# Optimization experiments

Measured on AMD Instinct MI355X. Metric: run time of the kernel, lower is better.

## Reference

```python
import jax, jax.numpy as jnp
import numpy as np

B = 16384
C = 2048  # in_channel
OUT = 2   # out_channel


def setup_inputs() -> dict:
    key = jax.random.key(0)
    k1, k2, k3, k4, k5, k6, k7 = jax.random.split(key, 7)
    scale = 1.0 / np.sqrt(3 * C)  # torch Linear default init range
    return {
        "s_f": jax.random.normal(k1, (B, C), dtype=jnp.float32),
        "g_f": jax.random.normal(k2, (B, C), dtype=jnp.float32),
        "v_f": jax.random.normal(k3, (B, C), dtype=jnp.float32),
        "W_aff": jax.random.uniform(k4, (3 * C, 3), dtype=jnp.float32, minval=-scale, maxval=scale),
        "b_aff": jax.random.uniform(k5, (3,), dtype=jnp.float32, minval=-scale, maxval=scale),
        "W_cls": jax.random.uniform(k6, (3 * C, OUT), dtype=jnp.float32, minval=-scale, maxval=scale),
        "b_cls": jax.random.uniform(k7, (OUT,), dtype=jnp.float32, minval=-scale, maxval=scale),
    }


def reference(s_f, g_f, v_f, W_aff, b_aff, W_cls, b_cls):
    # Attention gating over the three modalities.
    x_att = jnp.concatenate([s_f, g_f, v_f], axis=1)          # [B, 3C]
    att = jax.nn.softmax(x_att @ W_aff + b_aff, axis=1)       # [B, 3]
    # diag(att[:, i]) @ f  ==  per-row scalar scaling (broadcast multiply).
    s = att[:, 0:1] * s_f
    g = att[:, 1:2] * g_f
    v = att[:, 2:3] * v_f
    x = jnp.concatenate([s, g, v], axis=1)                    # [B, 3C]
    return jax.nn.softmax(x @ W_cls + b_cls, axis=1)          # [B, OUT]
```

## Files before the change

### kernel.cpp

```cpp
#include <hip/hip_runtime.h>

#define B_ROWS 16384
#define C_DIM  2048
#define BLK    256
#define CHUNK  8
#define RPB    32
#define GROUP  8

#define DPP_ADD(v, ctrl, rmask) \
  v += __int_as_float(__builtin_amdgcn_update_dpp(0, __float_as_int(v), (ctrl), (rmask), 0xf, false))

__device__ __forceinline__ float wave_sum64(float v) {
  DPP_ADD(v, 0x111, 0xf);
  DPP_ADD(v, 0x112, 0xf);
  DPP_ADD(v, 0x114, 0xf);
  DPP_ADD(v, 0x118, 0xf);
  DPP_ADD(v, 0x142, 0xa);
  DPP_ADD(v, 0x143, 0xc);
  return v;
}

__global__ __launch_bounds__(BLK, 2)
void maff_fused(const float* __restrict__ s_f,
                const float* __restrict__ g_f,
                const float* __restrict__ v_f,
                const float* __restrict__ W_aff,
                const float* __restrict__ b_aff,
                const float* __restrict__ W_cls,
                const float* __restrict__ b_cls,
                float* __restrict__ out)
{
  const int t    = threadIdx.x;
  const int lane = t & 63;
  const int wave = t >> 6;
  const int c0   = t * CHUNK;

  float wa[3][CHUNK][3];
  float wc[3][CHUNK][2];
#pragma unroll
  for (int m = 0; m < 3; ++m) {
#pragma unroll
    for (int i = 0; i < CHUNK; ++i) {
      const int cc = m * C_DIM + c0 + i;
      wa[m][i][0] = W_aff[cc * 3 + 0];
      wa[m][i][1] = W_aff[cc * 3 + 1];
      wa[m][i][2] = W_aff[cc * 3 + 2];
      wc[m][i][0] = W_cls[cc * 2 + 0];
      wc[m][i][1] = W_cls[cc * 2 + 1];
    }
  }
  const float ba0 = b_aff[0], ba1 = b_aff[1], ba2 = b_aff[2];
  const float bc0 = b_cls[0], bc1 = b_cls[1];

  __shared__ float red[2][GROUP][4][9];

  const int row0 = blockIdx.x * RPB;

  float4 cs0, cs1, cg0, cg1, cv0, cv1;
  {
    const size_t off = (size_t)row0 * C_DIM + c0;
    cs0 = *(const float4*)(s_f + off); cs1 = *(const float4*)(s_f + off + 4);
    cg0 = *(const float4*)(g_f + off); cg1 = *(const float4*)(g_f + off + 4);
    cv0 = *(const float4*)(v_f + off); cv1 = *(const float4*)(v_f + off + 4);
  }

  for (int r = 0; r < RPB; ++r) {
    const int    pr   = (r + 1 < RPB) ? (row0 + r + 1) : row0;
    const size_t poff = (size_t)pr * C_DIM + c0;
    float4 ns0 = *(const float4*)(s_f + poff);
    float4 ns1 = *(const float4*)(s_f + poff + 4);
    float4 ng0 = *(const float4*)(g_f + poff);
    float4 ng1 = *(const float4*)(g_f + poff + 4);
    float4 nv0 = *(const float4*)(v_f + poff);
    float4 nv1 = *(const float4*)(v_f + poff + 4);

    float fs[CHUNK], fg[CHUNK], fv[CHUNK];
    fs[0]=cs0.x; fs[1]=cs0.y; fs[2]=cs0.z; fs[3]=cs0.w;
    fs[4]=cs1.x; fs[5]=cs1.y; fs[6]=cs1.z; fs[7]=cs1.w;
    fg[0]=cg0.x; fg[1]=cg0.y; fg[2]=cg0.z; fg[3]=cg0.w;
    fg[4]=cg1.x; fg[5]=cg1.y; fg[6]=cg1.z; fg[7]=cg1.w;
    fv[0]=cv0.x; fv[1]=cv0.y; fv[2]=cv0.z; fv[3]=cv0.w;
    fv[4]=cv1.x; fv[5]=cv1.y; fv[6]=cv1.z; fv[7]=cv1.w;

    float a0=0.f, a1=0.f, a2=0.f;
    float d00=0.f, d01=0.f, d10=0.f, d11=0.f, d20=0.f, d21=0.f;
#pragma unroll
    for (int i = 0; i < CHUNK; ++i) {
      a0 = fmaf(fs[i], wa[0][i][0], a0);
      a1 = fmaf(fs[i], wa[0][i][1], a1);
      a2 = fmaf(fs[i], wa[0][i][2], a2);
      a0 = fmaf(fg[i], wa[1][i][0], a0);
      a1 = fmaf(fg[i], wa[1][i][1], a1);
      a2 = fmaf(fg[i], wa[1][i][2], a2);
      a0 = fmaf(fv[i], wa[2][i][0], a0);
      a1 = fmaf(fv[i], wa[2][i][1], a1);
      a2 = fmaf(fv[i], wa[2][i][2], a2);
      d00 = fmaf(fs[i], wc[0][i][0], d00);
      d01 = fmaf(fs[i], wc[0][i][1], d01);
      d10 = fmaf(fg[i], wc[1][i][0], d10);
      d11 = fmaf(fg[i], wc[1][i][1], d11);
      d20 = fmaf(fv[i], wc[2][i][0], d20);
      d21 = fmaf(fv[i], wc[2][i][1], d21);
    }

    a0  = wave_sum64(a0);  a1  = wave_sum64(a1);  a2  = wave_sum64(a2);
    d00 = wave_sum64(d00); d01 = wave_sum64(d01);
    d10 = wave_sum64(d10); d11 = wave_sum64(d11);
    d20 = wave_sum64(d20); d21 = wave_sum64(d21);

    const int gslot = r & (GROUP - 1);
    const int gbuf  = (r / GROUP) & 1;
    if (lane == 63) {
      float* dst = &red[gbuf][gslot][wave][0];
      dst[0] = a0;  dst[1] = a1;  dst[2] = a2;
      dst[3] = d00; dst[4] = d01; dst[5] = d10;
      dst[6] = d11; dst[7] = d20; dst[8] = d21;
    }

    if (gslot == GROUP - 1) {
      __syncthreads();
      if (t < GROUP) {
        const float* q = &red[gbuf][t][0][0];
        float A0  = q[0] + q[ 9] + q[18] + q[27] + ba0;
        float A1  = q[1] + q[10] + q[19] + q[28] + ba1;
        float A2  = q[2] + q[11] + q[20] + q[29] + ba2;
        float D00 = q[3] + q[12] + q[21] + q[30];
        float D01 = q[4] + q[13] + q[22] + q[31];
        float D10 = q[5] + q[14] + q[23] + q[32];
        float D11 = q[6] + q[15] + q[24] + q[33];
        float D20 = q[7] + q[16] + q[25] + q[34];
        float D21 = q[8] + q[17] + q[26] + q[35];

        float mx = fmaxf(A0, fmaxf(A1, A2));
        float e0 = __expf(A0 - mx), e1 = __expf(A1 - mx), e2 = __expf(A2 - mx);
        float inv = 1.0f / (e0 + e1 + e2);
        float t0 = e0 * inv, t1 = e1 * inv, t2 = e2 * inv;

        float L0 = t0 * D00 + t1 * D10 + t2 * D20 + bc0;
        float L1 = t0 * D01 + t1 * D11 + t2 * D21 + bc1;
        float mm = fmaxf(L0, L1);
        float x0 = __expf(L0 - mm), x1 = __expf(L1 - mm);
        float is = 1.0f / (x0 + x1);

        const int row = row0 + (r - (GROUP - 1)) + t;
        *(float2*)(out + (size_t)row * 2) = make_float2(x0 * is, x1 * is);
      }
    }

    cs0 = ns0; cs1 = ns1; cg0 = ng0; cg1 = ng1; cv0 = nv0; cv1 = nv1;
  }
}

extern "C" void kernel_launch(void* const* d_in, const int* in_sizes, int n_in,
                              void* d_out, int out_size, void* d_ws, size_t ws_size,
                              hipStream_t stream) {
  const float* s_f   = (const float*)d_in[0];
  const float* g_f   = (const float*)d_in[1];
  const float* v_f   = (const float*)d_in[2];
  const float* W_aff = (const float*)d_in[3];
  const float* b_aff = (const float*)d_in[4];
  const float* W_cls = (const float*)d_in[5];
  const float* b_cls = (const float*)d_in[6];
  float* out = (float*)d_out;

  dim3 grid(B_ROWS / RPB);
  dim3 block(BLK);
  maff_fused<<<grid, block, 0, stream>>>(s_f, g_f, v_f, W_aff, b_aff, W_cls, b_cls, out);
}
```

Measured before the change: 364.2 us.

## Use 512-thread blocks with 4-wide chunks and 16 rows per block

Doubles the block to 512 threads, so each thread covers 4 channels instead of 8, and halves the rows per block to 16, which doubles the grid. Weight loads become vectorized float4 reads, and the cross-wave reduction loops over 8 waves. The aim is higher occupancy and more memory-level parallelism for this bandwidth-bound streaming kernel. In exchange, per-wave shuffle reductions and block barriers double relative to the data each thread handles.

```diff
diff --git a/kernel.cpp b/kernel.cpp
--- a/kernel.cpp
+++ b/kernel.cpp
@@ -2,10 +2,11 @@
 
 #define B_ROWS 16384
 #define C_DIM  2048
-#define BLK    256
-#define CHUNK  8
-#define RPB    32
+#define BLK    512
+#define CHUNK  4
+#define RPB    16
 #define GROUP  8
+#define NWAVE  (BLK / 64)
 
 #define DPP_ADD(v, ctrl, rmask) \
   v += __int_as_float(__builtin_amdgcn_update_dpp(0, __float_as_int(v), (ctrl), (rmask), 0xf, false))
@@ -20,7 +21,7 @@
   return v;
 }
 
-__global__ __launch_bounds__(BLK, 2)
+__global__ __launch_bounds__(BLK, 4)
 void maff_fused(const float* __restrict__ s_f,
                 const float* __restrict__ g_f,
                 const float* __restrict__ v_f,
@@ -35,72 +36,65 @@
   const int wave = t >> 6;
   const int c0   = t * CHUNK;
 
-  float wa[3][CHUNK][3];
-  float wc[3][CHUNK][2];
+  float waf[3][12];
+  float wcf[3][8];
 #pragma unroll
   for (int m = 0; m < 3; ++m) {
-#pragma unroll
-    for (int i = 0; i < CHUNK; ++i) {
-      const int cc = m * C_DIM + c0 + i;
-      wa[m][i][0] = W_aff[cc * 3 + 0];
-      wa[m][i][1] = W_aff[cc * 3 + 1];
-      wa[m][i][2] = W_aff[cc * 3 + 2];
-      wc[m][i][0] = W_cls[cc * 2 + 0];
-      wc[m][i][1] = W_cls[cc * 2 + 1];
-    }
+    const float4* pa = (const float4*)(W_aff + (size_t)(m * C_DIM + c0) * 3);
+    float4 a0 = pa[0], a1 = pa[1], a2 = pa[2];
+    waf[m][0]=a0.x; waf[m][1]=a0.y; waf[m][2]=a0.z; waf[m][3]=a0.w;
+    waf[m][4]=a1.x; waf[m][5]=a1.y; waf[m][6]=a1.z; waf[m][7]=a1.w;
+    waf[m][8]=a2.x; waf[m][9]=a2.y; waf[m][10]=a2.z; waf[m][11]=a2.w;
+    const float4* pc = (const float4*)(W_cls + (size_t)(m * C_DIM + c0) * 2);
+    float4 q0 = pc[0], q1 = pc[1];
+    wcf[m][0]=q0.x; wcf[m][1]=q0.y; wcf[m][2]=q0.z; wcf[m][3]=q0.w;
+    wcf[m][4]=q1.x; wcf[m][5]=q1.y; wcf[m][6]=q1.z; wcf[m][7]=q1.w;
   }
   const float ba0 = b_aff[0], ba1 = b_aff[1], ba2 = b_aff[2];
   const float bc0 = b_cls[0], bc1 = b_cls[1];
 
-  __shared__ float red[2][GROUP][4][9];
+  __shared__ float red[2][GROUP][NWAVE][9];
 
   const int row0 = blockIdx.x * RPB;
 
-  float4 cs0, cs1, cg0, cg1, cv0, cv1;
+  float4 cs, cg, cv;
   {
     const size_t off = (size_t)row0 * C_DIM + c0;
-    cs0 = *(const float4*)(s_f + off); cs1 = *(const float4*)(s_f + off + 4);
-    cg0 = *(const float4*)(g_f + off); cg1 = *(const float4*)(g_f + off + 4);
-    cv0 = *(const float4*)(v_f + off); cv1 = *(const float4*)(v_f + off + 4);
+    cs = *(const float4*)(s_f + off);
+    cg = *(const float4*)(g_f + off);
+    cv = *(const float4*)(v_f + off);
   }
 
   for (int r = 0; r < RPB; ++r) {
-    const int    pr   = (r + 1 < RPB) ? (row0 + r + 1) : row0;
+    const int    pr   = row0 + ((r + 1 < RPB) ? (r + 1) : r);
     const size_t poff = (size_t)pr * C_DIM + c0;
-    float4 ns0 = *(const float4*)(s_f + poff);
-    float4 ns1 = *(const float4*)(s_f + poff + 4);
-    float4 ng0 = *(const float4*)(g_f + poff);
-    float4 ng1 = *(const float4*)(g_f + poff + 4);
-    float4 nv0 = *(const float4*)(v_f + poff);
-    float4 nv1 = *(const float4*)(v_f + poff + 4);
+    float4 ns = *(const float4*)(s_f + poff);
+    float4 ng = *(const float4*)(g_f + poff);
+    float4 nv = *(const float4*)(v_f + poff);
 
-    float fs[CHUNK], fg[CHUNK], fv[CHUNK];
-    fs[0]=cs0.x; fs[1]=cs0.y; fs[2]=cs0.z; fs[3]=cs0.w;
-    fs[4]=cs1.x; fs[5]=cs1.y; fs[6]=cs1.z; fs[7]=cs1.w;
-    fg[0]=cg0.x; fg[1]=cg0.y; fg[2]=cg0.z; fg[3]=cg0.w;
-    fg[4]=cg1.x; fg[5]=cg1.y; fg[6]=cg1.z; fg[7]=cg1.w;
-    fv[0]=cv0.x; fv[1]=cv0.y; fv[2]=cv0.z; fv[3]=cv0.w;
-    fv[4]=cv1.x; fv[5]=cv1.y; fv[6]=cv1.z; fv[7]=cv1.w;
+    float fs[CHUNK] = {cs.x, cs.y, cs.z, cs.w};
+    float fg[CHUNK] = {cg.x, cg.y, cg.z, cg.w};
+    float fv[CHUNK] = {cv.x, cv.y, cv.z, cv.w};
 
     float a0=0.f, a1=0.f, a2=0.f;
     float d00=0.f, d01=0.f, d10=0.f, d11=0.f, d20=0.f, d21=0.f;
 #pragma unroll
     for (int i = 0; i < CHUNK; ++i) {
-      a0 = fmaf(fs[i], wa[0][i][0], a0);
-      a1 = fmaf(fs[i], wa[0][i][1], a1);
-      a2 = fmaf(fs[i], wa[0][i][2], a2);
-      a0 = fmaf(fg[i], wa[1][i][0], a0);
-      a1 = fmaf(fg[i], wa[1][i][1], a1);
-      a2 = fmaf(fg[i], wa[1][i][2], a2);
-      a0 = fmaf(fv[i], wa[2][i][0], a0);
-      a1 = fmaf(fv[i], wa[2][i][1], a1);
-      a2 = fmaf(fv[i], wa[2][i][2], a2);
-      d00 = fmaf(fs[i], wc[0][i][0], d00);
-      d01 = fmaf(fs[i], wc[0][i][1], d01);
-      d10 = fmaf(fg[i], wc[1][i][0], d10);
-      d11 = fmaf(fg[i], wc[1][i][1], d11);
-      d20 = fmaf(fv[i], wc[2][i][0], d20);
-      d21 = fmaf(fv[i], wc[2][i][1], d21);
+      a0  = fmaf(fs[i], waf[0][i*3+0], a0);
+      a1  = fmaf(fs[i], waf[0][i*3+1], a1);
+      a2  = fmaf(fs[i], waf[0][i*3+2], a2);
+      a0  = fmaf(fg[i], waf[1][i*3+0], a0);
+      a1  = fmaf(fg[i], waf[1][i*3+1], a1);
+      a2  = fmaf(fg[i], waf[1][i*3+2], a2);
+      a0  = fmaf(fv[i], waf[2][i*3+0], a0);
+      a1  = fmaf(fv[i], waf[2][i*3+1], a1);
+      a2  = fmaf(fv[i], waf[2][i*3+2], a2);
+      d00 = fmaf(fs[i], wcf[0][i*2+0], d00);
+      d01 = fmaf(fs[i], wcf[0][i*2+1], d01);
+      d10 = fmaf(fg[i], wcf[1][i*2+0], d10);
+      d11 = fmaf(fg[i], wcf[1][i*2+1], d11);
+      d20 = fmaf(fv[i], wcf[2][i*2+0], d20);
+      d21 = fmaf(fv[i], wcf[2][i*2+1], d21);
     }
 
     a0  = wave_sum64(a0);  a1  = wave_sum64(a1);  a2  = wave_sum64(a2);
@@ -109,7 +103,7 @@
     d20 = wave_sum64(d20); d21 = wave_sum64(d21);
 
     const int gslot = r & (GROUP - 1);
-    const int gbuf  = (r / GROUP) & 1;
+    const int gbuf  = (r >> 3) & 1;
     if (lane == 63) {
       float* dst = &red[gbuf][gslot][wave][0];
       dst[0] = a0;  dst[1] = a1;  dst[2] = a2;
@@ -121,15 +115,15 @@
       __syncthreads();
       if (t < GROUP) {
         const float* q = &red[gbuf][t][0][0];
-        float A0  = q[0] + q[ 9] + q[18] + q[27] + ba0;
-        float A1  = q[1] + q[10] + q[19] + q[28] + ba1;
-        float A2  = q[2] + q[11] + q[20] + q[29] + ba2;
-        float D00 = q[3] + q[12] + q[21] + q[30];
-        float D01 = q[4] + q[13] + q[22] + q[31];
-        float D10 = q[5] + q[14] + q[23] + q[32];
-        float D11 = q[6] + q[15] + q[24] + q[33];
-        float D20 = q[7] + q[16] + q[25] + q[34];
-        float D21 = q[8] + q[17] + q[26] + q[35];
+        float A0=ba0, A1=ba1, A2=ba2;
+        float D00=0.f, D01=0.f, D10=0.f, D11=0.f, D20=0.f, D21=0.f;
+#pragma unroll
+        for (int w = 0; w < NWAVE; ++w) {
+          const float* p = q + w * 9;
+          A0 += p[0]; A1 += p[1]; A2 += p[2];
+          D00 += p[3]; D01 += p[4]; D10 += p[5];
+          D11 += p[6]; D20 += p[7]; D21 += p[8];
+        }
 
         float mx = fmaxf(A0, fmaxf(A1, A2));
         float e0 = __expf(A0 - mx), e1 = __expf(A1 - mx), e2 = __expf(A2 - mx);
@@ -147,7 +141,7 @@
       }
     }
 
-    cs0 = ns0; cs1 = ns1; cg0 = ng0; cg1 = ng1; cv0 = nv0; cv1 = nv1;
+    cs = ns; cg = ng; cv = nv;
   }
 }
 
```

Measured after the change: 378.5 us. 1.04x slower.
